# Kernel optimization log

Hardware: AMD Instinct MI355X
Metric: run time of the kernel (lower is better)

The kernel has to match this reference:

```python
import jax, jax.numpy as jnp
import numpy as np

EPS = 1e-5
NUM_HEADS = 8


def bn(x, gamma, beta, mean, var):
    # eval-mode BatchNorm2d over channel dim (NCHW)
    inv = gamma / jnp.sqrt(var + EPS)
    return x * inv[None, :, None, None] + (beta - mean * inv)[None, :, None, None]


def conv1x1(x, w):
    # w: (O, I, 1, 1) -> pointwise matmul
    return jnp.einsum('bchw,oc->bohw', x, w[:, :, 0, 0])


def conv3x3(x, w):
    return jax.lax.conv_general_dilated(
        x, w, window_strides=(1, 1), padding=((1, 1), (1, 1)),
        dimension_numbers=('NCHW', 'OIHW', 'NCHW'))


def setup_inputs() -> dict:
    key = jax.random.key(0)
    ks = jax.random.split(key, 4)
    B, C, H, W = 2, 256, 64, 64
    return {
        'x': jax.random.normal(ks[0], (B, C, H, W), jnp.float32),
        'w_qkv': jax.random.normal(ks[1], (3 * C, C, 1, 1), jnp.float32) * 0.05,
        'w_local': jax.random.normal(ks[2], (C, C, 3, 3), jnp.float32) * 0.05,
        'local_gamma': jnp.ones((C,), jnp.float32),
        'local_beta': jnp.zeros((C,), jnp.float32),
        'local_mean': jnp.zeros((C,), jnp.float32),
        'local_var': jnp.ones((C,), jnp.float32),
        'w_proj': jax.random.normal(ks[3], (C, C, 1, 1), jnp.float32) * 0.05,
        'proj_gamma': jnp.ones((C,), jnp.float32),
        'proj_beta': jnp.zeros((C,), jnp.float32),
        'proj_mean': jnp.zeros((C,), jnp.float32),
        'proj_var': jnp.ones((C,), jnp.float32),
    }


def reference(x, w_qkv, w_local, local_gamma, local_beta, local_mean, local_var,
              w_proj, proj_gamma, proj_beta, proj_mean, proj_var):
    B, C, H, W = x.shape
    hd = C // NUM_HEADS
    scale = hd ** -0.5
    # qkv: (B, 3C, H, W) -> (B, 3, heads, hd, N)
    qkv = conv1x1(x, w_qkv).reshape(B, 3, NUM_HEADS, hd, H * W)
    q, k, v = qkv[:, 0], qkv[:, 1], qkv[:, 2]  # each (B, heads, hd, N)
    attn = jnp.einsum('bhdn,bhdm->bhnm', q, k) * scale  # (B, heads, N, N)
    attn = jax.nn.softmax(attn, axis=-1)
    out = jnp.einsum('bhnm,bhdm->bhdn', attn, v).reshape(B, C, H, W)
    local_out = bn(conv3x3(x, w_local), local_gamma, local_beta, local_mean, local_var)
    return bn(conv1x1(out + local_out, w_proj), proj_gamma, proj_beta, proj_mean, proj_var)
```

## Files before the change

kernel.cpp:

```cpp
#include <hip/hip_runtime.h>

#define EPSV 1e-5f

typedef unsigned short u16;
typedef unsigned int u32;
typedef __attribute__((ext_vector_type(8))) short bf16x8;
typedef __attribute__((ext_vector_type(4))) float f32x4;

__device__ __forceinline__ u16 f2bf(float f) {
  u32 u = __float_as_uint(f);
  u32 r = (u + 0x7FFFu + ((u >> 16) & 1u)) >> 16;
  return (u16)r;
}
__device__ __forceinline__ float fexp2(float x) {
  float r;
  asm("v_exp_f32 %0, %1" : "=v"(r) : "v"(x));
  return r;
}

#define MFMA(a, b, c) __builtin_amdgcn_mfma_f32_16x16x32_bf16((a), (b), (c), 0, 0, 0)

__global__ __launch_bounds__(256) void prep_x_kernel(
    const float* __restrict__ x, u16* __restrict__ xT) {
  __shared__ float Ls[16][260];
  const int nt = blockIdx.x, cb = blockIdx.y, b = blockIdx.z;
  const int tid = threadIdx.x;
  const int cc0 = tid >> 6, n4 = (tid & 63) * 4;
  const float* xb = x + ((size_t)(b * 256 + cb * 16)) * 4096 + nt * 256;
#pragma unroll
  for (int j = 0; j < 4; j++) {
    int cc = j * 4 + cc0;
    *(float4*)&Ls[cc][n4] = *(const float4*)(xb + (size_t)cc * 4096 + n4);
  }
  __syncthreads();
  const int n = tid;
  u16 buf[16];
#pragma unroll
  for (int c = 0; c < 16; c++) buf[c] = f2bf(Ls[c][n]);
  u16* dst = xT + ((size_t)cb * 8192 + b * 4096 + nt * 256 + n) * 16;
  *(uint4*)(dst) = *(uint4*)&buf[0];
  *(uint4*)(dst + 8) = *(uint4*)&buf[8];
}

__global__ __launch_bounds__(256) void prep_w_kernel(
    const float* __restrict__ wqkv, const float* __restrict__ wproj,
    const float* __restrict__ wloc,
    u16* __restrict__ wqkvb, u16* __restrict__ wprojb, u16* __restrict__ wb) {
  const int bid = blockIdx.x, c = threadIdx.x;
  const float QSCALE = 0.17677669529663687f * 1.4426950408889634f;
  if (bid < 768) {
    float sc = (bid < 256) ? QSCALE : 1.0f;
    wqkvb[bid * 256 + c] = f2bf(wqkv[bid * 256 + c] * sc);
  } else if (bid < 1024) {
    int o = bid - 768;
    wprojb[o * 256 + c] = f2bf(wproj[o * 256 + c]);
  } else {
    int o = bid - 1024;
    const float* src = wloc + ((size_t)o * 256 + c) * 9;
#pragma unroll
    for (int tap = 0; tap < 9; tap++)
      wb[tap * 65536 + o * 256 + c] = f2bf(src[tap]);
  }
}

__global__ __launch_bounds__(256, 4) void qkv_mfma_kernel(
    const u16* __restrict__ xT, const u16* __restrict__ wqkvb,
    u16* __restrict__ Qg, u16* __restrict__ Kg, u16* __restrict__ Vtg) {
  const int nB = blockIdx.x * 128;
  const int oB = blockIdx.y * 64;
  const int tid = threadIdx.x, lane = tid & 63, wv = tid >> 6;
  const int n16 = lane & 15, G = lane >> 4;
  const int waveO = oB + (wv >> 1) * 32;
  const int waveN = nB + (wv & 1) * 64;
  f32x4 acc[2][4] = {};
  const u16* Ap = wqkvb + (size_t)(waveO + n16) * 256 + G * 8;
  const u16* Bp = xT + ((size_t)(G >> 1) * 8192 + waveN + n16) * 16 + (G & 1) * 8;
  for (int c0 = 0; c0 < 256; c0 += 32) {
    bf16x8 a0 = *(const bf16x8*)(Ap + c0);
    bf16x8 a1 = *(const bf16x8*)(Ap + 16 * 256 + c0);
    const u16* bp = Bp + (size_t)(c0 >> 4) * 131072;
    bf16x8 b0 = *(const bf16x8*)(bp);
    bf16x8 b1 = *(const bf16x8*)(bp + 256);
    bf16x8 b2 = *(const bf16x8*)(bp + 512);
    bf16x8 b3 = *(const bf16x8*)(bp + 768);
    acc[0][0] = MFMA(a0, b0, acc[0][0]);
    acc[0][1] = MFMA(a0, b1, acc[0][1]);
    acc[0][2] = MFMA(a0, b2, acc[0][2]);
    acc[0][3] = MFMA(a0, b3, acc[0][3]);
    acc[1][0] = MFMA(a1, b0, acc[1][0]);
    acc[1][1] = MFMA(a1, b1, acc[1][1]);
    acc[1][2] = MFMA(a1, b2, acc[1][2]);
    acc[1][3] = MFMA(a1, b3, acc[1][3]);
  }
  const int which = oB >> 8;
  if (which < 2) {
    u16* base = which ? Kg : Qg;
#pragma unroll
    for (int i = 0; i < 2; i++) {
      int o0 = waveO + i * 16 + G * 4;
      int h = (o0 >> 5) & 7, d0 = o0 & 31;
#pragma unroll
      for (int j = 0; j < 4; j++) {
        int s = waveN + j * 16 + n16;
        int b = s >> 12, n = s & 4095;
        u16 pk[4];
#pragma unroll
        for (int r = 0; r < 4; r++) pk[r] = f2bf(acc[i][j][r]);
        *(uint2*)(base + ((size_t)(b * 8 + h) * 4096 + n) * 32 + d0) = *(uint2*)pk;
      }
    }
  } else {
#pragma unroll
    for (int i = 0; i < 2; i++) {
      int o0 = waveO + i * 16 + G * 4;
      int h = (o0 >> 5) & 7, d0 = o0 & 31;
#pragma unroll
      for (int j = 0; j < 4; j++) {
        int s = waveN + j * 16 + n16;
        int b = s >> 12, n = s & 4095;
        u16* vp = Vtg + ((size_t)(b * 8 + h) * 32 + d0) * 4096 + n;
#pragma unroll
        for (int r = 0; r < 4; r++) vp[(size_t)r * 4096] = f2bf(acc[i][j][r]);
      }
    }
  }
}

__global__ __launch_bounds__(256, 4) void conv_mfma_kernel(
    const u16* __restrict__ xT, const u16* __restrict__ wb,
    const float* __restrict__ g, const float* __restrict__ be,
    const float* __restrict__ mu, const float* __restrict__ var,
    u16* __restrict__ localT) {
  const int nB = blockIdx.x * 64;
  const int oB = blockIdx.y * 64;
  const int tid = threadIdx.x, lane = tid & 63, wv = tid >> 6;
  const int n16 = lane & 15, G = lane >> 4;
  const int waveO = oB + (wv >> 1) * 32;
  const int waveN = nB + (wv & 1) * 32;
  const int y = (nB >> 6) & 63;
  const int x0 = waveN & 63;
  f32x4 acc[2][2] = {};
  const u16* Ap = wb + (size_t)(waveO + n16) * 256 + G * 8;
  const u16* Bp = xT + ((size_t)(G >> 1) * 8192 + waveN + n16) * 16 + (G & 1) * 8;
  const bf16x8 z = {0, 0, 0, 0, 0, 0, 0, 0};
  for (int c0 = 0; c0 < 256; c0 += 32) {
    const u16* bp = Bp + (size_t)(c0 >> 4) * 131072;
    const u16* ap = Ap + c0;
#pragma unroll
    for (int tap = 0; tap < 9; tap++) {
      const int dy = tap / 3 - 1, dx = tap % 3 - 1;
      int yy = y + dy;
      if ((unsigned)yy >= 64u) continue;
      bf16x8 a0 = *(const bf16x8*)(ap + (size_t)tap * 65536);
      bf16x8 a1 = *(const bf16x8*)(ap + (size_t)tap * 65536 + 16 * 256);
      const int off = dy * 64 + dx;
      bf16x8 b0, b1;
      if (dx == 0) {
        b0 = *(const bf16x8*)(bp + (ptrdiff_t)off * 16);
        b1 = *(const bf16x8*)(bp + (ptrdiff_t)(off + 16) * 16);
      } else {
        bool v0 = (unsigned)(x0 + n16 + dx) < 64u;
        bool v1 = (unsigned)(x0 + 16 + n16 + dx) < 64u;
        int o0 = v0 ? off : 0;
        int o1 = v1 ? (off + 16) : 16;
        bf16x8 t0 = *(const bf16x8*)(bp + (ptrdiff_t)o0 * 16);
        bf16x8 t1 = *(const bf16x8*)(bp + (ptrdiff_t)o1 * 16);
        b0 = v0 ? t0 : z;
        b1 = v1 ? t1 : z;
      }
      acc[0][0] = MFMA(a0, b0, acc[0][0]);
      acc[0][1] = MFMA(a0, b1, acc[0][1]);
      acc[1][0] = MFMA(a1, b0, acc[1][0]);
      acc[1][1] = MFMA(a1, b1, acc[1][1]);
    }
  }
#pragma unroll
  for (int i = 0; i < 2; i++) {
    int o0 = waveO + i * 16 + G * 4;
    float inv[4], sh[4];
#pragma unroll
    for (int r = 0; r < 4; r++) {
      int o = o0 + r;
      float iv = g[o] * rsqrtf(var[o] + EPSV);
      inv[r] = iv; sh[r] = be[o] - mu[o] * iv;
    }
#pragma unroll
    for (int j = 0; j < 2; j++) {
      int s = waveN + j * 16 + n16;
      u16 pk[4];
#pragma unroll
      for (int r = 0; r < 4; r++) pk[r] = f2bf(acc[i][j][r] * inv[r] + sh[r]);
      *(uint2*)(localT + ((size_t)(o0 >> 4) * 8192 + s) * 16 + (o0 & 15)) = *(uint2*)pk;
    }
  }
}

__global__ __launch_bounds__(256, 4) void flash_mfma_kernel(
    const u16* __restrict__ Qg, const u16* __restrict__ Kg,
    const u16* __restrict__ Vtg, u16* __restrict__ attnT) {
  __shared__ u32 Ps[4][32 * 36];
  __shared__ float MX[2][64][20];
  const int bid = blockIdx.x;
  const int bh = bid >> 6, qt = bid & 63;
  const int tid = threadIdx.x, lane = tid & 63, w = tid >> 6;
  const int n16 = lane & 15, G = lane >> 4;
  const int g = w >> 1, mh = w & 1;
  const int b = bh >> 3, h = bh & 7;
  const int qbase = qt * 64 + g * 32;

  const u16* Qp = Qg + ((size_t)bh * 4096 + qbase) * 32;
  const bf16x8 qf0 = *(const bf16x8*)(Qp + (size_t)n16 * 32 + G * 8);
  const bf16x8 qf1 = *(const bf16x8*)(Qp + (size_t)(16 + n16) * 32 + G * 8);

  f32x4 O00 = {0.f,0.f,0.f,0.f}, O01 = {0.f,0.f,0.f,0.f};
  f32x4 O10 = {0.f,0.f,0.f,0.f}, O11 = {0.f,0.f,0.f,0.f};
  float m0 = -3.0e38f, m1 = -3.0e38f, l0 = 0.f, l1 = 0.f;

  const u16* Kb = Kg + ((size_t)bh * 4096 + mh * 2048) * 32;
  const u16* Vb = Vtg + (size_t)bh * 32 * 4096 + mh * 2048;
  u32* Pw = Ps[w];

  for (int it = 0; it < 32; ++it) {
    const u16* Kt = Kb + (size_t)it * 64 * 32;
    bf16x8 kf0 = *(const bf16x8*)(Kt + (size_t)(n16) * 32 + G * 8);
    bf16x8 kf1 = *(const bf16x8*)(Kt + (size_t)(16 + n16) * 32 + G * 8);
    bf16x8 kf2 = *(const bf16x8*)(Kt + (size_t)(32 + n16) * 32 + G * 8);
    bf16x8 kf3 = *(const bf16x8*)(Kt + (size_t)(48 + n16) * 32 + G * 8);
    const f32x4 z = {0.f, 0.f, 0.f, 0.f};
    f32x4 S0[4], S1[4];
    S0[0] = MFMA(kf0, qf0, z);
    S0[1] = MFMA(kf1, qf0, z);
    S0[2] = MFMA(kf2, qf0, z);
    S0[3] = MFMA(kf3, qf0, z);
    S1[0] = MFMA(kf0, qf1, z);
    S1[1] = MFMA(kf1, qf1, z);
    S1[2] = MFMA(kf2, qf1, z);
    S1[3] = MFMA(kf3, qf1, z);

    float mt0 = fmaxf(fmaxf(S0[0].x, S0[0].y), fmaxf(S0[0].z, S0[0].w));
    float mt1 = fmaxf(fmaxf(S1[0].x, S1[0].y), fmaxf(S1[0].z, S1[0].w));
#pragma unroll
    for (int t = 1; t < 4; t++) {
      mt0 = fmaxf(mt0, fmaxf(fmaxf(S0[t].x, S0[t].y), fmaxf(S0[t].z, S0[t].w)));
      mt1 = fmaxf(mt1, fmaxf(fmaxf(S1[t].x, S1[t].y), fmaxf(S1[t].z, S1[t].w)));
    }
    mt0 = fmaxf(mt0, __shfl_xor(mt0, 16, 64));
    mt0 = fmaxf(mt0, __shfl_xor(mt0, 32, 64));
    mt1 = fmaxf(mt1, __shfl_xor(mt1, 16, 64));
    mt1 = fmaxf(mt1, __shfl_xor(mt1, 32, 64));
    float mn0 = fmaxf(m0, mt0), mn1 = fmaxf(m1, mt1);
    if (__any((mt0 > m0) | (mt1 > m1))) {
      float a0 = fexp2(m0 - mn0);
      float a1 = fexp2(m1 - mn1);
      l0 *= a0; l1 *= a1;
      O00 *= a0; O01 *= a0; O10 *= a1; O11 *= a1;
    }
    m0 = mn0; m1 = mn1;

    float rs0 = 0.f, rs1 = 0.f;
#pragma unroll
    for (int t = 0; t < 4; t++) {
      float p0 = fexp2(S0[t].x - m0);
      float p1 = fexp2(S0[t].y - m0);
      float p2 = fexp2(S0[t].z - m0);
      float p3 = fexp2(S0[t].w - m0);
      rs0 += (p0 + p1) + (p2 + p3);
      uint2 pr;
      pr.x = __builtin_amdgcn_perm(__float_as_uint(p1), __float_as_uint(p0), 0x07060302u);
      pr.y = __builtin_amdgcn_perm(__float_as_uint(p3), __float_as_uint(p2), 0x07060302u);
      *(uint2*)&Pw[n16 * 36 + 8 * t + 2 * G] = pr;
      float q0 = fexp2(S1[t].x - m1);
      float q1 = fexp2(S1[t].y - m1);
      float q2 = fexp2(S1[t].z - m1);
      float q3 = fexp2(S1[t].w - m1);
      rs1 += (q0 + q1) + (q2 + q3);
      uint2 qr;
      qr.x = __builtin_amdgcn_perm(__float_as_uint(q1), __float_as_uint(q0), 0x07060302u);
      qr.y = __builtin_amdgcn_perm(__float_as_uint(q3), __float_as_uint(q2), 0x07060302u);
      *(uint2*)&Pw[(16 + n16) * 36 + 8 * t + 2 * G] = qr;
    }
    rs0 += __shfl_xor(rs0, 16, 64);
    rs0 += __shfl_xor(rs0, 32, 64);
    rs1 += __shfl_xor(rs1, 16, 64);
    rs1 += __shfl_xor(rs1, 32, 64);
    l0 += rs0; l1 += rs1;

#pragma unroll
    for (int c = 0; c < 2; c++) {
      const u16* Vp = Vb + (size_t)it * 64 + c * 32 + G * 8;
      bf16x8 va0 = *(const bf16x8*)(Vp + (size_t)n16 * 4096);
      bf16x8 va1 = *(const bf16x8*)(Vp + (size_t)(16 + n16) * 4096);
      union { uint4 u; bf16x8 v; } B0, B1;
      B0.u = *(uint4*)&Pw[n16 * 36 + 16 * c + 4 * G];
      B1.u = *(uint4*)&Pw[(16 + n16) * 36 + 16 * c + 4 * G];
      O00 = MFMA(va0, B0.v, O00);
      O01 = MFMA(va1, B0.v, O01);
      O10 = MFMA(va0, B1.v, O10);
      O11 = MFMA(va1, B1.v, O11);
    }
  }

  if (mh == 1) {
    float* dst = &MX[g][lane][0];
    *(f32x4*)(dst + 0)  = O00;
    *(f32x4*)(dst + 4)  = O01;
    *(f32x4*)(dst + 8)  = O10;
    *(f32x4*)(dst + 12) = O11;
    dst[16] = m0; dst[17] = l0; dst[18] = m1; dst[19] = l1;
  }
  __syncthreads();
  if (mh == 0) {
    const float* src = &MX[g][lane][0];
    f32x4 P00 = *(const f32x4*)(src + 0);
    f32x4 P01 = *(const f32x4*)(src + 4);
    f32x4 P10 = *(const f32x4*)(src + 8);
    f32x4 P11 = *(const f32x4*)(src + 12);
    float pm0 = src[16], pl0 = src[17], pm1 = src[18], pl1 = src[19];

    float M0 = fmaxf(m0, pm0);
    float se0 = fexp2(m0 - M0), so0 = fexp2(pm0 - M0);
    float rl0 = 1.0f / (l0 * se0 + pl0 * so0);
    float M1 = fmaxf(m1, pm1);
    float se1 = fexp2(m1 - M1), so1 = fexp2(pm1 - M1);
    float rl1 = 1.0f / (l1 * se1 + pl1 * so1);
    const int s0 = b * 4096 + qbase + n16;
    const int s1 = s0 + 16;
    const int cb0 = h * 2, cb1 = h * 2 + 1;
    u16 pk[4];
#pragma unroll
    for (int r = 0; r < 4; r++) pk[r] = f2bf((O00[r] * se0 + P00[r] * so0) * rl0);
    *(uint2*)(attnT + ((size_t)cb0 * 8192 + s0) * 16 + G * 4) = *(uint2*)pk;
#pragma unroll
    for (int r = 0; r < 4; r++) pk[r] = f2bf((O01[r] * se0 + P01[r] * so0) * rl0);
    *(uint2*)(attnT + ((size_t)cb1 * 8192 + s0) * 16 + G * 4) = *(uint2*)pk;
#pragma unroll
    for (int r = 0; r < 4; r++) pk[r] = f2bf((O10[r] * se1 + P10[r] * so1) * rl1);
    *(uint2*)(attnT + ((size_t)cb0 * 8192 + s1) * 16 + G * 4) = *(uint2*)pk;
#pragma unroll
    for (int r = 0; r < 4; r++) pk[r] = f2bf((O11[r] * se1 + P11[r] * so1) * rl1);
    *(uint2*)(attnT + ((size_t)cb1 * 8192 + s1) * 16 + G * 4) = *(uint2*)pk;
  }
}

__global__ __launch_bounds__(256, 4) void proj_mfma_kernel(
    const u16* __restrict__ attnT, const u16* __restrict__ localT,
    const u16* __restrict__ wprojb,
    const float* __restrict__ g, const float* __restrict__ be,
    const float* __restrict__ mu, const float* __restrict__ var,
    float* __restrict__ out) {
  const int nB = blockIdx.x * 64;
  const int oB = blockIdx.y * 64;
  const int tid = threadIdx.x, lane = tid & 63, wv = tid >> 6;
  const int n16 = lane & 15, G = lane >> 4;
  const int waveO = oB + (wv >> 1) * 32;
  const int waveN = nB + (wv & 1) * 32;
  f32x4 acc[2][2] = {};
  const u16* Ap = wprojb + (size_t)(waveO + n16) * 256 + G * 8;
  const size_t boff = ((size_t)(G >> 1) * 8192 + waveN + n16) * 16 + (G & 1) * 8;
  for (int c0 = 0; c0 < 256; c0 += 32) {
    bf16x8 a0 = *(const bf16x8*)(Ap + c0);
    bf16x8 a1 = *(const bf16x8*)(Ap + 16 * 256 + c0);
    const size_t bo = boff + (size_t)(c0 >> 4) * 131072;
    bf16x8 p0 = *(const bf16x8*)(attnT + bo);
    bf16x8 p1 = *(const bf16x8*)(attnT + bo + 256);
    bf16x8 q0 = *(const bf16x8*)(localT + bo);
    bf16x8 q1 = *(const bf16x8*)(localT + bo + 256);
    acc[0][0] = MFMA(a0, p0, acc[0][0]);
    acc[0][1] = MFMA(a0, p1, acc[0][1]);
    acc[1][0] = MFMA(a1, p0, acc[1][0]);
    acc[1][1] = MFMA(a1, p1, acc[1][1]);
    acc[0][0] = MFMA(a0, q0, acc[0][0]);
    acc[0][1] = MFMA(a0, q1, acc[0][1]);
    acc[1][0] = MFMA(a1, q0, acc[1][0]);
    acc[1][1] = MFMA(a1, q1, acc[1][1]);
  }
#pragma unroll
  for (int i = 0; i < 2; i++) {
    int o0 = waveO + i * 16 + G * 4;
    float inv[4], sh[4];
#pragma unroll
    for (int r = 0; r < 4; r++) {
      int o = o0 + r;
      float iv = g[o] * rsqrtf(var[o] + EPSV);
      inv[r] = iv; sh[r] = be[o] - mu[o] * iv;
    }
#pragma unroll
    for (int j = 0; j < 2; j++) {
      int s = waveN + j * 16 + n16;
      int b = s >> 12, n = s & 4095;
      float* op = out + ((size_t)(b * 256 + o0)) * 4096 + n;
#pragma unroll
      for (int r = 0; r < 4; r++) op[(size_t)r * 4096] = acc[i][j][r] * inv[r] + sh[r];
    }
  }
}

extern "C" void kernel_launch(void* const* d_in, const int* in_sizes, int n_in,
                              void* d_out, int out_size, void* d_ws, size_t ws_size,
                              hipStream_t stream) {
  (void)in_sizes; (void)n_in; (void)out_size; (void)ws_size;
  const float* x       = (const float*)d_in[0];
  const float* w_qkv   = (const float*)d_in[1];
  const float* w_local = (const float*)d_in[2];
  const float* lg = (const float*)d_in[3];
  const float* lb = (const float*)d_in[4];
  const float* lm = (const float*)d_in[5];
  const float* lv = (const float*)d_in[6];
  const float* w_proj  = (const float*)d_in[7];
  const float* pg = (const float*)d_in[8];
  const float* pb = (const float*)d_in[9];
  const float* pm = (const float*)d_in[10];
  const float* pvr = (const float*)d_in[11];
  float* out = (float*)d_out;

  u16* Q      = (u16*)d_ws;
  u16* K      = Q + 2097152;
  u16* Vt     = K + 2097152;
  u16* xT     = Vt + 2097152;
  u16* attnT  = xT + 2097152;
  u16* localT = attnT + 2097152;
  u16* wqkvb  = localT + 2097152;
  u16* wprojb = wqkvb + 196608;
  u16* wb     = wprojb + 65536;

  hipLaunchKernelGGL(prep_x_kernel, dim3(16, 16, 2), dim3(256), 0, stream, x, xT);
  hipLaunchKernelGGL(prep_w_kernel, dim3(1280), dim3(256), 0, stream,
                     w_qkv, w_proj, w_local, wqkvb, wprojb, wb);
  hipLaunchKernelGGL(qkv_mfma_kernel, dim3(64, 12), dim3(256), 0, stream,
                     xT, wqkvb, Q, K, Vt);
  hipLaunchKernelGGL(conv_mfma_kernel, dim3(128, 4), dim3(256), 0, stream,
                     xT, wb, lg, lb, lm, lv, localT);
  hipLaunchKernelGGL(flash_mfma_kernel, dim3(1024), dim3(256), 0, stream,
                     Q, K, Vt, attnT);
  hipLaunchKernelGGL(proj_mfma_kernel, dim3(128, 4), dim3(256), 0, stream,
                     attnT, localT, wprojb, pg, pb, pm, pvr, out);
}
```

Before: 239.2 us.

## Merge prep and qkv/conv launches, prefetch K tiles, defer row-sum reduction

Folds the two prep kernels into one launch and the QKV projection and 3x3 conv into one launch using block-index ranges, which cuts launch count and lets the conv and QKV blocks share the GPU concurrently. In the flash attention loop, the next K tile is loaded right after the QK MFMAs so the load overlaps the softmax work. The per-iteration cross-lane row-sum shuffles are replaced by per-lane partial sums that are reduced once at the end. The fused kernel carries the register needs of both branches, which may lower occupancy, and the K prefetch adds live registers.

```diff
diff --git a/kernel.cpp b/kernel.cpp
--- a/kernel.cpp
+++ b/kernel.cpp
@@ -20,177 +20,178 @@
 
 #define MFMA(a, b, c) __builtin_amdgcn_mfma_f32_16x16x32_bf16((a), (b), (c), 0, 0, 0)
 
-__global__ __launch_bounds__(256) void prep_x_kernel(
-    const float* __restrict__ x, u16* __restrict__ xT) {
+__global__ __launch_bounds__(256) void prep_kernel(
+    const float* __restrict__ x, const float* __restrict__ wqkv,
+    const float* __restrict__ wproj, const float* __restrict__ wloc,
+    u16* __restrict__ xT, u16* __restrict__ wqkvb,
+    u16* __restrict__ wprojb, u16* __restrict__ wb) {
   __shared__ float Ls[16][260];
-  const int nt = blockIdx.x, cb = blockIdx.y, b = blockIdx.z;
+  const int bid = blockIdx.x;
   const int tid = threadIdx.x;
-  const int cc0 = tid >> 6, n4 = (tid & 63) * 4;
-  const float* xb = x + ((size_t)(b * 256 + cb * 16)) * 4096 + nt * 256;
-#pragma unroll
-  for (int j = 0; j < 4; j++) {
-    int cc = j * 4 + cc0;
-    *(float4*)&Ls[cc][n4] = *(const float4*)(xb + (size_t)cc * 4096 + n4);
-  }
-  __syncthreads();
-  const int n = tid;
-  u16 buf[16];
-#pragma unroll
-  for (int c = 0; c < 16; c++) buf[c] = f2bf(Ls[c][n]);
-  u16* dst = xT + ((size_t)cb * 8192 + b * 4096 + nt * 256 + n) * 16;
-  *(uint4*)(dst) = *(uint4*)&buf[0];
-  *(uint4*)(dst + 8) = *(uint4*)&buf[8];
-}
-
-__global__ __launch_bounds__(256) void prep_w_kernel(
-    const float* __restrict__ wqkv, const float* __restrict__ wproj,
-    const float* __restrict__ wloc,
-    u16* __restrict__ wqkvb, u16* __restrict__ wprojb, u16* __restrict__ wb) {
-  const int bid = blockIdx.x, c = threadIdx.x;
-  const float QSCALE = 0.17677669529663687f * 1.4426950408889634f;
-  if (bid < 768) {
-    float sc = (bid < 256) ? QSCALE : 1.0f;
-    wqkvb[bid * 256 + c] = f2bf(wqkv[bid * 256 + c] * sc);
-  } else if (bid < 1024) {
-    int o = bid - 768;
-    wprojb[o * 256 + c] = f2bf(wproj[o * 256 + c]);
+  if (bid < 512) {
+    const int nt = bid & 15, cb = (bid >> 4) & 15, b = bid >> 8;
+    const int cc0 = tid >> 6, n4 = (tid & 63) * 4;
+    const float* xb = x + ((size_t)(b * 256 + cb * 16)) * 4096 + nt * 256;
+#pragma unroll
+    for (int j = 0; j < 4; j++) {
+      int cc = j * 4 + cc0;
+      *(float4*)&Ls[cc][n4] = *(const float4*)(xb + (size_t)cc * 4096 + n4);
+    }
+    __syncthreads();
+    const int n = tid;
+    u16 buf[16];
+#pragma unroll
+    for (int c = 0; c < 16; c++) buf[c] = f2bf(Ls[c][n]);
+    u16* dst = xT + ((size_t)cb * 8192 + b * 4096 + nt * 256 + n) * 16;
+    *(uint4*)(dst) = *(uint4*)&buf[0];
+    *(uint4*)(dst + 8) = *(uint4*)&buf[8];
   } else {
-    int o = bid - 1024;
-    const float* src = wloc + ((size_t)o * 256 + c) * 9;
-#pragma unroll
-    for (int tap = 0; tap < 9; tap++)
-      wb[tap * 65536 + o * 256 + c] = f2bf(src[tap]);
-  }
-}
-
-__global__ __launch_bounds__(256, 4) void qkv_mfma_kernel(
+    const int r = bid - 512, c = tid;
+    const float QSCALE = 0.17677669529663687f * 1.4426950408889634f;
+    if (r < 768) {
+      float sc = (r < 256) ? QSCALE : 1.0f;
+      wqkvb[r * 256 + c] = f2bf(wqkv[r * 256 + c] * sc);
+    } else if (r < 1024) {
+      int o = r - 768;
+      wprojb[o * 256 + c] = f2bf(wproj[o * 256 + c]);
+    } else {
+      int o = r - 1024;
+      const float* src = wloc + ((size_t)o * 256 + c) * 9;
+#pragma unroll
+      for (int tap = 0; tap < 9; tap++)
+        wb[tap * 65536 + o * 256 + c] = f2bf(src[tap]);
+    }
+  }
+}
+
+__global__ __launch_bounds__(256, 4) void qkvconv_kernel(
     const u16* __restrict__ xT, const u16* __restrict__ wqkvb,
-    u16* __restrict__ Qg, u16* __restrict__ Kg, u16* __restrict__ Vtg) {
-  const int nB = blockIdx.x * 128;
-  const int oB = blockIdx.y * 64;
+    const u16* __restrict__ wb,
+    const float* __restrict__ g, const float* __restrict__ be,
+    const float* __restrict__ mu, const float* __restrict__ var,
+    u16* __restrict__ Qg, u16* __restrict__ Kg, u16* __restrict__ Vtg,
+    u16* __restrict__ localT) {
+  const int bid = blockIdx.x;
   const int tid = threadIdx.x, lane = tid & 63, wv = tid >> 6;
   const int n16 = lane & 15, G = lane >> 4;
-  const int waveO = oB + (wv >> 1) * 32;
-  const int waveN = nB + (wv & 1) * 64;
-  f32x4 acc[2][4] = {};
-  const u16* Ap = wqkvb + (size_t)(waveO + n16) * 256 + G * 8;
-  const u16* Bp = xT + ((size_t)(G >> 1) * 8192 + waveN + n16) * 16 + (G & 1) * 8;
-  for (int c0 = 0; c0 < 256; c0 += 32) {
-    bf16x8 a0 = *(const bf16x8*)(Ap + c0);
-    bf16x8 a1 = *(const bf16x8*)(Ap + 16 * 256 + c0);
-    const u16* bp = Bp + (size_t)(c0 >> 4) * 131072;
-    bf16x8 b0 = *(const bf16x8*)(bp);
-    bf16x8 b1 = *(const bf16x8*)(bp + 256);
-    bf16x8 b2 = *(const bf16x8*)(bp + 512);
-    bf16x8 b3 = *(const bf16x8*)(bp + 768);
-    acc[0][0] = MFMA(a0, b0, acc[0][0]);
-    acc[0][1] = MFMA(a0, b1, acc[0][1]);
-    acc[0][2] = MFMA(a0, b2, acc[0][2]);
-    acc[0][3] = MFMA(a0, b3, acc[0][3]);
-    acc[1][0] = MFMA(a1, b0, acc[1][0]);
-    acc[1][1] = MFMA(a1, b1, acc[1][1]);
-    acc[1][2] = MFMA(a1, b2, acc[1][2]);
-    acc[1][3] = MFMA(a1, b3, acc[1][3]);
-  }
-  const int which = oB >> 8;
-  if (which < 2) {
-    u16* base = which ? Kg : Qg;
+  if (bid < 768) {
+    const int nB = (bid & 63) * 128;
+    const int oB = (bid >> 6) * 64;
+    const int waveO = oB + (wv >> 1) * 32;
+    const int waveN = nB + (wv & 1) * 64;
+    f32x4 acc[2][4] = {};
+    const u16* Ap = wqkvb + (size_t)(waveO + n16) * 256 + G * 8;
+    const u16* Bp = xT + ((size_t)(G >> 1) * 8192 + waveN + n16) * 16 + (G & 1) * 8;
+    for (int c0 = 0; c0 < 256; c0 += 32) {
+      bf16x8 a0 = *(const bf16x8*)(Ap + c0);
+      bf16x8 a1 = *(const bf16x8*)(Ap + 16 * 256 + c0);
+      const u16* bp = Bp + (size_t)(c0 >> 4) * 131072;
+      bf16x8 b0 = *(const bf16x8*)(bp);
+      bf16x8 b1 = *(const bf16x8*)(bp + 256);
+      bf16x8 b2 = *(const bf16x8*)(bp + 512);
+      bf16x8 b3 = *(const bf16x8*)(bp + 768);
+      acc[0][0] = MFMA(a0, b0, acc[0][0]);
+      acc[0][1] = MFMA(a0, b1, acc[0][1]);
+      acc[0][2] = MFMA(a0, b2, acc[0][2]);
+      acc[0][3] = MFMA(a0, b3, acc[0][3]);
+      acc[1][0] = MFMA(a1, b0, acc[1][0]);
+      acc[1][1] = MFMA(a1, b1, acc[1][1]);
+      acc[1][2] = MFMA(a1, b2, acc[1][2]);
+      acc[1][3] = MFMA(a1, b3, acc[1][3]);
+    }
+    const int which = oB >> 8;
+    if (which < 2) {
+      u16* base = which ? Kg : Qg;
+#pragma unroll
+      for (int i = 0; i < 2; i++) {
+        int o0 = waveO + i * 16 + G * 4;
+        int h = (o0 >> 5) & 7, d0 = o0 & 31;
+#pragma unroll
+        for (int j = 0; j < 4; j++) {
+          int s = waveN + j * 16 + n16;
+          int b = s >> 12, n = s & 4095;
+          u16 pk[4];
+#pragma unroll
+          for (int r = 0; r < 4; r++) pk[r] = f2bf(acc[i][j][r]);
+          *(uint2*)(base + ((size_t)(b * 8 + h) * 4096 + n) * 32 + d0) = *(uint2*)pk;
+        }
+      }
+    } else {
+#pragma unroll
+      for (int i = 0; i < 2; i++) {
+        int o0 = waveO + i * 16 + G * 4;
+        int h = (o0 >> 5) & 7, d0 = o0 & 31;
+#pragma unroll
+        for (int j = 0; j < 4; j++) {
+          int s = waveN + j * 16 + n16;
+          int b = s >> 12, n = s & 4095;
+          u16* vp = Vtg + ((size_t)(b * 8 + h) * 32 + d0) * 4096 + n;
+#pragma unroll
+          for (int r = 0; r < 4; r++) vp[(size_t)r * 4096] = f2bf(acc[i][j][r]);
+        }
+      }
+    }
+  } else {
+    const int r0 = bid - 768;
+    const int nB = (r0 & 127) * 64;
+    const int oB = (r0 >> 7) * 64;
+    const int waveO = oB + (wv >> 1) * 32;
+    const int waveN = nB + (wv & 1) * 32;
+    const int y = (nB >> 6) & 63;
+    const int x0 = waveN & 63;
+    f32x4 acc[2][2] = {};
+    const u16* Ap = wb + (size_t)(waveO + n16) * 256 + G * 8;
+    const u16* Bp = xT + ((size_t)(G >> 1) * 8192 + waveN + n16) * 16 + (G & 1) * 8;
+    const bf16x8 z = {0, 0, 0, 0, 0, 0, 0, 0};
+    for (int c0 = 0; c0 < 256; c0 += 32) {
+      const u16* bp = Bp + (size_t)(c0 >> 4) * 131072;
+      const u16* ap = Ap + c0;
+#pragma unroll
+      for (int tap = 0; tap < 9; tap++) {
+        const int dy = tap / 3 - 1, dx = tap % 3 - 1;
+        int yy = y + dy;
+        if ((unsigned)yy >= 64u) continue;
+        bf16x8 a0 = *(const bf16x8*)(ap + (size_t)tap * 65536);
+        bf16x8 a1 = *(const bf16x8*)(ap + (size_t)tap * 65536 + 16 * 256);
+        const int off = dy * 64 + dx;
+        bf16x8 b0, b1;
+        if (dx == 0) {
+          b0 = *(const bf16x8*)(bp + (ptrdiff_t)off * 16);
+          b1 = *(const bf16x8*)(bp + (ptrdiff_t)(off + 16) * 16);
+        } else {
+          bool v0 = (unsigned)(x0 + n16 + dx) < 64u;
+          bool v1 = (unsigned)(x0 + 16 + n16 + dx) < 64u;
+          int o0 = v0 ? off : 0;
+          int o1 = v1 ? (off + 16) : 16;
+          bf16x8 t0 = *(const bf16x8*)(bp + (ptrdiff_t)o0 * 16);
+          bf16x8 t1 = *(const bf16x8*)(bp + (ptrdiff_t)o1 * 16);
+          b0 = v0 ? t0 : z;
+          b1 = v1 ? t1 : z;
+        }
+        acc[0][0] = MFMA(a0, b0, acc[0][0]);
+        acc[0][1] = MFMA(a0, b1, acc[0][1]);
+        acc[1][0] = MFMA(a1, b0, acc[1][0]);
+        acc[1][1] = MFMA(a1, b1, acc[1][1]);
+      }
+    }
 #pragma unroll
     for (int i = 0; i < 2; i++) {
       int o0 = waveO + i * 16 + G * 4;
-      int h = (o0 >> 5) & 7, d0 = o0 & 31;
-#pragma unroll
-      for (int j = 0; j < 4; j++) {
+      float inv[4], sh[4];
+#pragma unroll
+      for (int r = 0; r < 4; r++) {
+        int o = o0 + r;
+        float iv = g[o] * rsqrtf(var[o] + EPSV);
+        inv[r] = iv; sh[r] = be[o] - mu[o] * iv;
+      }
+#pragma unroll
+      for (int j = 0; j < 2; j++) {
         int s = waveN + j * 16 + n16;
-        int b = s >> 12, n = s & 4095;
         u16 pk[4];
 #pragma unroll
-        for (int r = 0; r < 4; r++) pk[r] = f2bf(acc[i][j][r]);
-        *(uint2*)(base + ((size_t)(b * 8 + h) * 4096 + n) * 32 + d0) = *(uint2*)pk;
+        for (int r = 0; r < 4; r++) pk[r] = f2bf(acc[i][j][r] * inv[r] + sh[r]);
+        *(uint2*)(localT + ((size_t)(o0 >> 4) * 8192 + s) * 16 + (o0 & 15)) = *(uint2*)pk;
       }
-    }
-  } else {
-#pragma unroll
-    for (int i = 0; i < 2; i++) {
-      int o0 = waveO + i * 16 + G * 4;
-      int h = (o0 >> 5) & 7, d0 = o0 & 31;
-#pragma unroll
-      for (int j = 0; j < 4; j++) {
-        int s = waveN + j * 16 + n16;
-        int b = s >> 12, n = s & 4095;
-        u16* vp = Vtg + ((size_t)(b * 8 + h) * 32 + d0) * 4096 + n;
-#pragma unroll
-        for (int r = 0; r < 4; r++) vp[(size_t)r * 4096] = f2bf(acc[i][j][r]);
-      }
-    }
-  }
-}
-
-__global__ __launch_bounds__(256, 4) void conv_mfma_kernel(
-    const u16* __restrict__ xT, const u16* __restrict__ wb,
-    const float* __restrict__ g, const float* __restrict__ be,
-    const float* __restrict__ mu, const float* __restrict__ var,
-    u16* __restrict__ localT) {
-  const int nB = blockIdx.x * 64;
-  const int oB = blockIdx.y * 64;
-  const int tid = threadIdx.x, lane = tid & 63, wv = tid >> 6;
-  const int n16 = lane & 15, G = lane >> 4;
-  const int waveO = oB + (wv >> 1) * 32;
-  const int waveN = nB + (wv & 1) * 32;
-  const int y = (nB >> 6) & 63;
-  const int x0 = waveN & 63;
-  f32x4 acc[2][2] = {};
-  const u16* Ap = wb + (size_t)(waveO + n16) * 256 + G * 8;
-  const u16* Bp = xT + ((size_t)(G >> 1) * 8192 + waveN + n16) * 16 + (G & 1) * 8;
-  const bf16x8 z = {0, 0, 0, 0, 0, 0, 0, 0};
-  for (int c0 = 0; c0 < 256; c0 += 32) {
-    const u16* bp = Bp + (size_t)(c0 >> 4) * 131072;
-    const u16* ap = Ap + c0;
-#pragma unroll
-    for (int tap = 0; tap < 9; tap++) {
-      const int dy = tap / 3 - 1, dx = tap % 3 - 1;
-      int yy = y + dy;
-      if ((unsigned)yy >= 64u) continue;
-      bf16x8 a0 = *(const bf16x8*)(ap + (size_t)tap * 65536);
-      bf16x8 a1 = *(const bf16x8*)(ap + (size_t)tap * 65536 + 16 * 256);
-      const int off = dy * 64 + dx;
-      bf16x8 b0, b1;
-      if (dx == 0) {
-        b0 = *(const bf16x8*)(bp + (ptrdiff_t)off * 16);
-        b1 = *(const bf16x8*)(bp + (ptrdiff_t)(off + 16) * 16);
-      } else {
-        bool v0 = (unsigned)(x0 + n16 + dx) < 64u;
-        bool v1 = (unsigned)(x0 + 16 + n16 + dx) < 64u;
-        int o0 = v0 ? off : 0;
-        int o1 = v1 ? (off + 16) : 16;
-        bf16x8 t0 = *(const bf16x8*)(bp + (ptrdiff_t)o0 * 16);
-        bf16x8 t1 = *(const bf16x8*)(bp + (ptrdiff_t)o1 * 16);
-        b0 = v0 ? t0 : z;
-        b1 = v1 ? t1 : z;
-      }
-      acc[0][0] = MFMA(a0, b0, acc[0][0]);
-      acc[0][1] = MFMA(a0, b1, acc[0][1]);
-      acc[1][0] = MFMA(a1, b0, acc[1][0]);
-      acc[1][1] = MFMA(a1, b1, acc[1][1]);
-    }
-  }
-#pragma unroll
-  for (int i = 0; i < 2; i++) {
-    int o0 = waveO + i * 16 + G * 4;
-    float inv[4], sh[4];
-#pragma unroll
-    for (int r = 0; r < 4; r++) {
-      int o = o0 + r;
-      float iv = g[o] * rsqrtf(var[o] + EPSV);
-      inv[r] = iv; sh[r] = be[o] - mu[o] * iv;
-    }
-#pragma unroll
-    for (int j = 0; j < 2; j++) {
-      int s = waveN + j * 16 + n16;
-      u16 pk[4];
-#pragma unroll
-      for (int r = 0; r < 4; r++) pk[r] = f2bf(acc[i][j][r] * inv[r] + sh[r]);
-      *(uint2*)(localT + ((size_t)(o0 >> 4) * 8192 + s) * 16 + (o0 & 15)) = *(uint2*)pk;
     }
   }
 }
@@ -220,22 +221,26 @@
   const u16* Vb = Vtg + (size_t)bh * 32 * 4096 + mh * 2048;
   u32* Pw = Ps[w];
 
+  bf16x8 kf0 = *(const bf16x8*)(Kb + (size_t)n16 * 32 + G * 8);
+  bf16x8 kf1 = *(const bf16x8*)(Kb + (size_t)(16 + n16) * 32 + G * 8);
+  bf16x8 kf2 = *(const bf16x8*)(Kb + (size_t)(32 + n16) * 32 + G * 8);
+  bf16x8 kf3 = *(const bf16x8*)(Kb + (size_t)(48 + n16) * 32 + G * 8);
+
   for (int it = 0; it < 32; ++it) {
-    const u16* Kt = Kb + (size_t)it * 64 * 32;
-    bf16x8 kf0 = *(const bf16x8*)(Kt + (size_t)(n16) * 32 + G * 8);
-    bf16x8 kf1 = *(const bf16x8*)(Kt + (size_t)(16 + n16) * 32 + G * 8);
-    bf16x8 kf2 = *(const bf16x8*)(Kt + (size_t)(32 + n16) * 32 + G * 8);
-    bf16x8 kf3 = *(const bf16x8*)(Kt + (size_t)(48 + n16) * 32 + G * 8);
     const f32x4 z = {0.f, 0.f, 0.f, 0.f};
     f32x4 S0[4], S1[4];
-    S0[0] = MFMA(kf0, qf0, z);
-    S0[1] = MFMA(kf1, qf0, z);
-    S0[2] = MFMA(kf2, qf0, z);
-    S0[3] = MFMA(kf3, qf0, z);
-    S1[0] = MFMA(kf0, qf1, z);
-    S1[1] = MFMA(kf1, qf1, z);
-    S1[2] = MFMA(kf2, qf1, z);
-    S1[3] = MFMA(kf3, qf1, z);
+    S0[0] = MFMA(kf0, qf0, z); S1[0] = MFMA(kf0, qf1, z);
+    S0[1] = MFMA(kf1, qf0, z); S1[1] = MFMA(kf1, qf1, z);
+    S0[2] = MFMA(kf2, qf0, z); S1[2] = MFMA(kf2, qf1, z);
+    S0[3] = MFMA(kf3, qf0, z); S1[3] = MFMA(kf3, qf1, z);
+
+    {
+      const u16* Kn = Kb + (size_t)(((it + 1) & 31) * 64) * 32;
+      kf0 = *(const bf16x8*)(Kn + (size_t)n16 * 32 + G * 8);
+      kf1 = *(const bf16x8*)(Kn + (size_t)(16 + n16) * 32 + G * 8);
+      kf2 = *(const bf16x8*)(Kn + (size_t)(32 + n16) * 32 + G * 8);
+      kf3 = *(const bf16x8*)(Kn + (size_t)(48 + n16) * 32 + G * 8);
+    }
 
     float mt0 = fmaxf(fmaxf(S0[0].x, S0[0].y), fmaxf(S0[0].z, S0[0].w));
     float mt1 = fmaxf(fmaxf(S1[0].x, S1[0].y), fmaxf(S1[0].z, S1[0].w));
@@ -257,33 +262,23 @@
     }
     m0 = mn0; m1 = mn1;
 
-    float rs0 = 0.f, rs1 = 0.f;
 #pragma unroll
     for (int t = 0; t < 4; t++) {
-      float p0 = fexp2(S0[t].x - m0);
-      float p1 = fexp2(S0[t].y - m0);
-      float p2 = fexp2(S0[t].z - m0);
-      float p3 = fexp2(S0[t].w - m0);
-      rs0 += (p0 + p1) + (p2 + p3);
+      float p0 = fexp2(S0[t].x - m0), p1 = fexp2(S0[t].y - m0);
+      float p2 = fexp2(S0[t].z - m0), p3 = fexp2(S0[t].w - m0);
+      l0 += (p0 + p1) + (p2 + p3);
       uint2 pr;
       pr.x = __builtin_amdgcn_perm(__float_as_uint(p1), __float_as_uint(p0), 0x07060302u);
       pr.y = __builtin_amdgcn_perm(__float_as_uint(p3), __float_as_uint(p2), 0x07060302u);
       *(uint2*)&Pw[n16 * 36 + 8 * t + 2 * G] = pr;
-      float q0 = fexp2(S1[t].x - m1);
-      float q1 = fexp2(S1[t].y - m1);
-      float q2 = fexp2(S1[t].z - m1);
-      float q3 = fexp2(S1[t].w - m1);
-      rs1 += (q0 + q1) + (q2 + q3);
+      float q0 = fexp2(S1[t].x - m1), q1 = fexp2(S1[t].y - m1);
+      float q2 = fexp2(S1[t].z - m1), q3 = fexp2(S1[t].w - m1);
+      l1 += (q0 + q1) + (q2 + q3);
       uint2 qr;
       qr.x = __builtin_amdgcn_perm(__float_as_uint(q1), __float_as_uint(q0), 0x07060302u);
       qr.y = __builtin_amdgcn_perm(__float_as_uint(q3), __float_as_uint(q2), 0x07060302u);
       *(uint2*)&Pw[(16 + n16) * 36 + 8 * t + 2 * G] = qr;
     }
-    rs0 += __shfl_xor(rs0, 16, 64);
-    rs0 += __shfl_xor(rs0, 32, 64);
-    rs1 += __shfl_xor(rs1, 16, 64);
-    rs1 += __shfl_xor(rs1, 32, 64);
-    l0 += rs0; l1 += rs1;
 
 #pragma unroll
     for (int c = 0; c < 2; c++) {
@@ -319,10 +314,16 @@
 
     float M0 = fmaxf(m0, pm0);
     float se0 = fexp2(m0 - M0), so0 = fexp2(pm0 - M0);
-    float rl0 = 1.0f / (l0 * se0 + pl0 * so0);
     float M1 = fmaxf(m1, pm1);
     float se1 = fexp2(m1 - M1), so1 = fexp2(pm1 - M1);
-    float rl1 = 1.0f / (l1 * se1 + pl1 * so1);
+    float ls0 = l0 * se0 + pl0 * so0;
+    float ls1 = l1 * se1 + pl1 * so1;
+    ls0 += __shfl_xor(ls0, 16, 64);
+    ls0 += __shfl_xor(ls0, 32, 64);
+    ls1 += __shfl_xor(ls1, 16, 64);
+    ls1 += __shfl_xor(ls1, 32, 64);
+    const float rl0 = 1.0f / ls0, rl1 = 1.0f / ls1;
+
     const int s0 = b * 4096 + qbase + n16;
     const int s1 = s0 + 16;
     const int cb0 = h * 2, cb1 = h * 2 + 1;
@@ -423,13 +424,10 @@
   u16* wprojb = wqkvb + 196608;
   u16* wb     = wprojb + 65536;
 
-  hipLaunchKernelGGL(prep_x_kernel, dim3(16, 16, 2), dim3(256), 0, stream, x, xT);
-  hipLaunchKernelGGL(prep_w_kernel, dim3(1280), dim3(256), 0, stream,
-                     w_qkv, w_proj, w_local, wqkvb, wprojb, wb);
-  hipLaunchKernelGGL(qkv_mfma_kernel, dim3(64, 12), dim3(256), 0, stream,
-                     xT, wqkvb, Q, K, Vt);
-  hipLaunchKernelGGL(conv_mfma_kernel, dim3(128, 4), dim3(256), 0, stream,
-                     xT, wb, lg, lb, lm, lv, localT);
+  hipLaunchKernelGGL(prep_kernel, dim3(1792), dim3(256), 0, stream,
+                     x, w_qkv, w_proj, w_local, xT, wqkvb, wprojb, wb);
+  hipLaunchKernelGGL(qkvconv_kernel, dim3(1280), dim3(256), 0, stream,
+                     xT, wqkvb, wb, lg, lb, lm, lv, Q, K, Vt, localT);
   hipLaunchKernelGGL(flash_mfma_kernel, dim3(1024), dim3(256), 0, stream,
                      Q, K, Vt, attnT);
   hipLaunchKernelGGL(proj_mfma_kernel, dim3(128, 4), dim3(256), 0, stream,
```

Result: no change. 236.2 us (-1.3%).
